# Kernel tuning notes

Measured on AMD Instinct MI355X. Metric: run time of the kernel, lower is better.

The kernel has to match this reference:

```python
import jax, jax.numpy as jnp
import numpy as np

N = 4096
IN_DIM = 8
OUT_DIM = 8
MAX_DEPTH = 8


def _linear_params(key, fan_in, fan_out):
    kw, kb = jax.random.split(key)
    scale = 1.0 / np.sqrt(fan_in)
    W = jax.random.uniform(kw, (fan_in, fan_out), jnp.float32, -scale, scale)
    b = jax.random.uniform(kb, (fan_out,), jnp.float32, -scale, scale)
    return W, b


def setup_inputs() -> dict:
    key = jax.random.key(0)
    ks = jax.random.split(key, 8)
    x = jax.random.normal(ks[0], (N, IN_DIM), jnp.float32)
    # reachability matrices; scaled by 1/N to keep depth iteration stable
    rem = jax.random.uniform(ks[1], (MAX_DEPTH, N, N), jnp.float32) * (1.0 / N)
    pW1, pb1 = _linear_params(ks[2], IN_DIM, 16)
    pW2, pb2 = _linear_params(ks[3], 16, 8)
    pW3, pb3 = _linear_params(ks[4], 8, OUT_DIM)
    aW1, ab1 = _linear_params(ks[5], IN_DIM, 16)
    aW2, ab2 = _linear_params(ks[6], 16, 8)
    aW3, ab3 = _linear_params(ks[7], 8, OUT_DIM)
    return {
        "x": x, "reachable_edge_matrix": rem,
        "pW1": pW1, "pb1": pb1, "pW2": pW2, "pb2": pb2, "pW3": pW3, "pb3": pb3,
        "aW1": aW1, "ab1": ab1, "aW2": aW2, "ab2": ab2, "aW3": aW3, "ab3": ab3,
    }


def _mlp3(h, W1, b1, W2, b2, W3, b3):
    act = jax.nn.leaky_relu
    h = act(h @ W1 + b1)
    h = act(h @ W2 + b2)
    return act(h @ W3 + b3)


def reference(x, reachable_edge_matrix,
              pW1, pb1, pW2, pb2, pW3, pb3,
              aW1, ab1, aW2, ab2, aW3, ab3):
    out0 = _mlp3(x, pW1, pb1, pW2, pb2, pW3, pb3)  # [N, OUT_DIM]

    def step(out, A_d):
        agg = _mlp3(out, aW1, ab1, aW2, ab2, aW3, ab3)
        out = A_d @ agg + out  # [N,N]x[N,OUT_DIM] aggregation
        return out, None

    out, _ = jax.lax.scan(step, out0, reachable_edge_matrix)
    return out
```

## Files before the change

kernel.cpp:

```cpp
#include <hip/hip_runtime.h>

#define NN 4096

__device__ float g_outf[NN*8];
__device__ float g_agg0[NN*8];
__device__ float g_agg1[NN*8];

__device__ __forceinline__ float lrelu(float x){ return x > 0.0f ? x : 0.01f * x; }

__device__ void mlp3(const float* in,
                     const float* W1, const float* b1,
                     const float* W2, const float* b2,
                     const float* W3, const float* b3, float* out)
{
  float h1[16];
  #pragma unroll
  for (int m=0;m<16;m++){
    float s = b1[m];
    #pragma unroll
    for (int k=0;k<8;k++) s += in[k]*W1[k*16+m];
    h1[m] = lrelu(s);
  }
  float h2[8];
  #pragma unroll
  for (int m=0;m<8;m++){
    float s = b2[m];
    #pragma unroll
    for (int k=0;k<16;k++) s += h1[k]*W2[k*8+m];
    h2[m] = lrelu(s);
  }
  #pragma unroll
  for (int c=0;c<8;c++){
    float s = b3[c];
    #pragma unroll
    for (int k=0;k<8;k++) s += h2[k]*W3[k*8+c];
    out[c] = lrelu(s);
  }
}

__global__ __launch_bounds__(256) void init_kernel(
    const float* __restrict__ x,
    const float* pW1,const float* pb1,const float* pW2,const float* pb2,const float* pW3,const float* pb3,
    const float* aW1,const float* ab1,const float* aW2,const float* ab2,const float* aW3,const float* ab3)
{
  int i = blockIdx.x*256 + threadIdx.x;
  float in[8];
  #pragma unroll
  for (int k=0;k<8;k++) in[k] = x[i*8+k];
  float o[8];
  mlp3(in, pW1,pb1,pW2,pb2,pW3,pb3, o);
  #pragma unroll
  for (int c=0;c<8;c++) g_outf[i*8+c] = o[c];
  float a[8];
  mlp3(o, aW1,ab1,aW2,ab2,aW3,ab3, a);
  #pragma unroll
  for (int c=0;c<8;c++) g_agg0[i*8+c] = a[c];
}

__global__ __launch_bounds__(256,1) void agg_update(
    const float* __restrict__ A, int parity, float* __restrict__ finout,
    const float* __restrict__ aW1,const float* __restrict__ ab1,
    const float* __restrict__ aW2,const float* __restrict__ ab2,
    const float* __restrict__ aW3,const float* __restrict__ ab3)
{
  const float* aggin  = parity ? g_agg1 : g_agg0;
  float*       aggout = parity ? g_agg0 : g_agg1;

  const int lane = threadIdx.x & 63;
  const int wav  = threadIdx.x >> 6;
  const int i0   = (blockIdx.x*4 + wav) * 4;

  const float4* Ar0 = reinterpret_cast<const float4*>(A + (size_t)(i0+0)*NN) + lane;
  const float4* Ar1 = reinterpret_cast<const float4*>(A + (size_t)(i0+1)*NN) + lane;
  const float4* Ar2 = reinterpret_cast<const float4*>(A + (size_t)(i0+2)*NN) + lane;
  const float4* Ar3 = reinterpret_cast<const float4*>(A + (size_t)(i0+3)*NN) + lane;
  const float4* gp  = reinterpret_cast<const float4*>(aggin) + (size_t)lane*8;

  float acc[4][8];
  #pragma unroll
  for (int r=0;r<4;r++)
    #pragma unroll
    for (int c=0;c<8;c++) acc[r][c] = 0.0f;

  for (int it=0; it<16; ++it){
    float4 a0 = Ar0[it*64];
    float4 a1 = Ar1[it*64];
    float4 a2 = Ar2[it*64];
    float4 a3 = Ar3[it*64];
    float4 g[8];
    #pragma unroll
    for (int t=0;t<8;t++) g[t] = gp[it*512 + t];

    const float av[4][4] = {{a0.x,a0.y,a0.z,a0.w},
                            {a1.x,a1.y,a1.z,a1.w},
                            {a2.x,a2.y,a2.z,a2.w},
                            {a3.x,a3.y,a3.z,a3.w}};
    #pragma unroll
    for (int jj=0;jj<4;jj++){
      const float gl[8] = {g[2*jj].x, g[2*jj].y, g[2*jj].z, g[2*jj].w,
                           g[2*jj+1].x, g[2*jj+1].y, g[2*jj+1].z, g[2*jj+1].w};
      #pragma unroll
      for (int r=0;r<4;r++){
        const float a = av[r][jj];
        #pragma unroll
        for (int c=0;c<8;c++) acc[r][c] += a*gl[c];
      }
    }
  }

  #pragma unroll
  for (int r=0;r<4;r++)
    #pragma unroll
    for (int c=0;c<8;c++){
      float v = acc[r][c];
      #pragma unroll
      for (int s=1;s<64;s<<=1) v += __shfl_xor(v, s, 64);
      acc[r][c] = v;
    }

  const int r = lane >> 4, m = lane & 15;
  float* po = g_outf + (size_t)i0*8;

  float rowv[8];
  #pragma unroll
  for (int k=0;k<8;k++) rowv[k] = po[r*8+k] + acc[r][k];

  if (lane < 32){
    float t = 0.0f;
    #pragma unroll
    for (int rr=0;rr<4;rr++)
      #pragma unroll
      for (int cc=0;cc<8;cc++)
        if (rr*8+cc == lane) t = acc[rr][cc];
    float sv = po[lane] + t;
    po[lane] = sv;
    if (finout) finout[(size_t)i0*8 + lane] = sv;
  }

  if (!finout){
    float h1 = ab1[m];
    #pragma unroll
    for (int k=0;k<8;k++) h1 += rowv[k]*aW1[k*16+m];
    h1 = lrelu(h1);
    const int m8 = m & 7;
    float s2 = ab2[m8];
    #pragma unroll
    for (int k=0;k<16;k++) s2 += __shfl(h1, (lane & 48)+k, 64) * aW2[k*8+m8];
    float h2 = lrelu(s2);
    float s3 = ab3[m8];
    #pragma unroll
    for (int k=0;k<8;k++) s3 += __shfl(h2, (lane & 48)+k, 64) * aW3[k*8+m8];
    float av = lrelu(s3);
    if (m < 8) aggout[(size_t)(i0+r)*8 + m] = av;
  }
}

extern "C" void kernel_launch(void* const* d_in, const int* in_sizes, int n_in,
                              void* d_out, int out_size, void* d_ws, size_t ws_size,
                              hipStream_t stream)
{
  const float* x   = (const float*)d_in[0];
  const float* rem = (const float*)d_in[1];
  const float* pW1 = (const float*)d_in[2];
  const float* pb1 = (const float*)d_in[3];
  const float* pW2 = (const float*)d_in[4];
  const float* pb2 = (const float*)d_in[5];
  const float* pW3 = (const float*)d_in[6];
  const float* pb3 = (const float*)d_in[7];
  const float* aW1 = (const float*)d_in[8];
  const float* ab1 = (const float*)d_in[9];
  const float* aW2 = (const float*)d_in[10];
  const float* ab2 = (const float*)d_in[11];
  const float* aW3 = (const float*)d_in[12];
  const float* ab3 = (const float*)d_in[13];
  float* outf = (float*)d_out;

  init_kernel<<<16,256,0,stream>>>(x,pW1,pb1,pW2,pb2,pW3,pb3,
                                   aW1,ab1,aW2,ab2,aW3,ab3);
  for (int d=0; d<8; ++d){
    agg_update<<<256,256,0,stream>>>(rem + (size_t)d*NN*NN, (d&1),
                                     (d==7)? outf : (float*)nullptr,
                                     aW1,ab1,aW2,ab2,aW3,ab3);
  }
}
```

Baseline: 828.4 us.

## Fuse init and all depth steps into one persistent kernel with grid barrier

Replaces the init launch plus eight per-depth launches with a single persistent kernel of 256 blocks that synchronises between depth steps through a software sense-reversing grid barrier built on global atomics. It also register-prefetches the next A tile inside the loop and the first tile of the next depth, to hide load latency. This removes launch gaps and pipeline drain between steps. It relies on all 256 blocks being co-resident, otherwise it can deadlock. The barrier spin and fences add their own overhead, and the workload is dominated by streaming the 512MB A matrix from memory.

```diff
diff --git a/kernel.cpp b/kernel.cpp
--- a/kernel.cpp
+++ b/kernel.cpp
@@ -5,6 +5,8 @@
 __device__ float g_outf[NN*8];
 __device__ float g_agg0[NN*8];
 __device__ float g_agg1[NN*8];
+__device__ unsigned g_bar;
+__device__ unsigned g_sense;
 
 __device__ __forceinline__ float lrelu(float x){ return x > 0.0f ? x : 0.01f * x; }
 
@@ -38,120 +40,165 @@
   }
 }
 
-__global__ __launch_bounds__(256) void init_kernel(
-    const float* __restrict__ x,
-    const float* pW1,const float* pb1,const float* pW2,const float* pb2,const float* pW3,const float* pb3,
-    const float* aW1,const float* ab1,const float* aW2,const float* ab2,const float* aW3,const float* ab3)
-{
-  int i = blockIdx.x*256 + threadIdx.x;
-  float in[8];
-  #pragma unroll
-  for (int k=0;k<8;k++) in[k] = x[i*8+k];
-  float o[8];
-  mlp3(in, pW1,pb1,pW2,pb2,pW3,pb3, o);
-  #pragma unroll
-  for (int c=0;c<8;c++) g_outf[i*8+c] = o[c];
-  float a[8];
-  mlp3(o, aW1,ab1,aW2,ab2,aW3,ab3, a);
-  #pragma unroll
-  for (int c=0;c<8;c++) g_agg0[i*8+c] = a[c];
-}
-
-__global__ __launch_bounds__(256,1) void agg_update(
-    const float* __restrict__ A, int parity, float* __restrict__ finout,
+__device__ __forceinline__ void grid_sync()
+{
+  __threadfence();
+  __syncthreads();
+  if (threadIdx.x == 0){
+    unsigned gen = __hip_atomic_load(&g_sense, __ATOMIC_ACQUIRE, __HIP_MEMORY_SCOPE_AGENT);
+    unsigned n   = __hip_atomic_fetch_add(&g_bar, 1u, __ATOMIC_ACQ_REL, __HIP_MEMORY_SCOPE_AGENT);
+    if (n == gridDim.x - 1u){
+      __hip_atomic_store(&g_bar, 0u, __ATOMIC_RELAXED, __HIP_MEMORY_SCOPE_AGENT);
+      __hip_atomic_store(&g_sense, gen + 1u, __ATOMIC_RELEASE, __HIP_MEMORY_SCOPE_AGENT);
+    } else {
+      while (__hip_atomic_load(&g_sense, __ATOMIC_ACQUIRE, __HIP_MEMORY_SCOPE_AGENT) == gen)
+        __builtin_amdgcn_s_sleep(2);
+    }
+  }
+  __syncthreads();
+  __threadfence();
+}
+
+__global__ __launch_bounds__(256,1) void fused_graph(
+    const float* __restrict__ x, const float* __restrict__ rem,
+    float* __restrict__ finout,
+    const float* __restrict__ pW1,const float* __restrict__ pb1,
+    const float* __restrict__ pW2,const float* __restrict__ pb2,
+    const float* __restrict__ pW3,const float* __restrict__ pb3,
     const float* __restrict__ aW1,const float* __restrict__ ab1,
     const float* __restrict__ aW2,const float* __restrict__ ab2,
     const float* __restrict__ aW3,const float* __restrict__ ab3)
 {
-  const float* aggin  = parity ? g_agg1 : g_agg0;
-  float*       aggout = parity ? g_agg0 : g_agg1;
-
   const int lane = threadIdx.x & 63;
   const int wav  = threadIdx.x >> 6;
   const int i0   = (blockIdx.x*4 + wav) * 4;
 
-  const float4* Ar0 = reinterpret_cast<const float4*>(A + (size_t)(i0+0)*NN) + lane;
-  const float4* Ar1 = reinterpret_cast<const float4*>(A + (size_t)(i0+1)*NN) + lane;
-  const float4* Ar2 = reinterpret_cast<const float4*>(A + (size_t)(i0+2)*NN) + lane;
-  const float4* Ar3 = reinterpret_cast<const float4*>(A + (size_t)(i0+3)*NN) + lane;
-  const float4* gp  = reinterpret_cast<const float4*>(aggin) + (size_t)lane*8;
-
-  float acc[4][8];
-  #pragma unroll
-  for (int r=0;r<4;r++)
-    #pragma unroll
-    for (int c=0;c<8;c++) acc[r][c] = 0.0f;
-
-  for (int it=0; it<16; ++it){
-    float4 a0 = Ar0[it*64];
-    float4 a1 = Ar1[it*64];
-    float4 a2 = Ar2[it*64];
-    float4 a3 = Ar3[it*64];
-    float4 g[8];
-    #pragma unroll
-    for (int t=0;t<8;t++) g[t] = gp[it*512 + t];
-
-    const float av[4][4] = {{a0.x,a0.y,a0.z,a0.w},
-                            {a1.x,a1.y,a1.z,a1.w},
-                            {a2.x,a2.y,a2.z,a2.w},
-                            {a3.x,a3.y,a3.z,a3.w}};
-    #pragma unroll
-    for (int jj=0;jj<4;jj++){
-      const float gl[8] = {g[2*jj].x, g[2*jj].y, g[2*jj].z, g[2*jj].w,
-                           g[2*jj+1].x, g[2*jj+1].y, g[2*jj+1].z, g[2*jj+1].w};
-      #pragma unroll
-      for (int r=0;r<4;r++){
-        const float a = av[r][jj];
+  const float4* A0p = reinterpret_cast<const float4*>(rem + (size_t)(i0+0)*NN) + lane;
+  const float4* A1p = reinterpret_cast<const float4*>(rem + (size_t)(i0+1)*NN) + lane;
+  const float4* A2p = reinterpret_cast<const float4*>(rem + (size_t)(i0+2)*NN) + lane;
+  const float4* A3p = reinterpret_cast<const float4*>(rem + (size_t)(i0+3)*NN) + lane;
+
+  float4 nA0 = A0p[0], nA1 = A1p[0], nA2 = A2p[0], nA3 = A3p[0];
+
+  if (blockIdx.x < 16){
+    const int i = blockIdx.x*256 + threadIdx.x;
+    float in[8];
+    #pragma unroll
+    for (int k=0;k<8;k++) in[k] = x[i*8+k];
+    float o[8];
+    mlp3(in, pW1,pb1,pW2,pb2,pW3,pb3, o);
+    #pragma unroll
+    for (int c=0;c<8;c++) g_outf[i*8+c] = o[c];
+    float a[8];
+    mlp3(o, aW1,ab1,aW2,ab2,aW3,ab3, a);
+    #pragma unroll
+    for (int c=0;c<8;c++) g_agg0[i*8+c] = a[c];
+  }
+  grid_sync();
+
+  const size_t DSTEP = (size_t)NN*(NN/4);
+
+  for (int d=0; d<8; ++d){
+    const float* aggin  = (d&1) ? g_agg1 : g_agg0;
+    float*       aggout = (d&1) ? g_agg0 : g_agg1;
+    const float4* gp  = reinterpret_cast<const float4*>(aggin) + (size_t)lane*8;
+    const float4* Ad0 = A0p + (size_t)d*DSTEP;
+    const float4* Ad1 = A1p + (size_t)d*DSTEP;
+    const float4* Ad2 = A2p + (size_t)d*DSTEP;
+    const float4* Ad3 = A3p + (size_t)d*DSTEP;
+
+    float acc[4][8];
+    #pragma unroll
+    for (int r=0;r<4;r++)
+      #pragma unroll
+      for (int c=0;c<8;c++) acc[r][c] = 0.0f;
+
+    float4 cA0=nA0, cA1=nA1, cA2=nA2, cA3=nA3;
+
+    for (int it=0; it<16; ++it){
+      float4 fA0, fA1, fA2, fA3;
+      if (it < 15){
+        fA0 = Ad0[(it+1)*64];
+        fA1 = Ad1[(it+1)*64];
+        fA2 = Ad2[(it+1)*64];
+        fA3 = Ad3[(it+1)*64];
+      }
+      float4 G[8];
+      #pragma unroll
+      for (int t=0;t<8;t++) G[t] = gp[(size_t)it*512 + t];
+
+      const float av[4][4] = {{cA0.x,cA0.y,cA0.z,cA0.w},
+                              {cA1.x,cA1.y,cA1.z,cA1.w},
+                              {cA2.x,cA2.y,cA2.z,cA2.w},
+                              {cA3.x,cA3.y,cA3.z,cA3.w}};
+      #pragma unroll
+      for (int jj=0;jj<4;jj++){
+        const float gl[8] = {G[2*jj].x, G[2*jj].y, G[2*jj].z, G[2*jj].w,
+                             G[2*jj+1].x, G[2*jj+1].y, G[2*jj+1].z, G[2*jj+1].w};
         #pragma unroll
-        for (int c=0;c<8;c++) acc[r][c] += a*gl[c];
+        for (int r=0;r<4;r++){
+          const float a = av[r][jj];
+          #pragma unroll
+          for (int c=0;c<8;c++) acc[r][c] += a*gl[c];
+        }
       }
-    }
-  }
-
-  #pragma unroll
-  for (int r=0;r<4;r++)
-    #pragma unroll
-    for (int c=0;c<8;c++){
-      float v = acc[r][c];
-      #pragma unroll
-      for (int s=1;s<64;s<<=1) v += __shfl_xor(v, s, 64);
-      acc[r][c] = v;
-    }
-
-  const int r = lane >> 4, m = lane & 15;
-  float* po = g_outf + (size_t)i0*8;
-
-  float rowv[8];
-  #pragma unroll
-  for (int k=0;k<8;k++) rowv[k] = po[r*8+k] + acc[r][k];
-
-  if (lane < 32){
-    float t = 0.0f;
-    #pragma unroll
-    for (int rr=0;rr<4;rr++)
-      #pragma unroll
-      for (int cc=0;cc<8;cc++)
-        if (rr*8+cc == lane) t = acc[rr][cc];
-    float sv = po[lane] + t;
-    po[lane] = sv;
-    if (finout) finout[(size_t)i0*8 + lane] = sv;
-  }
-
-  if (!finout){
-    float h1 = ab1[m];
-    #pragma unroll
-    for (int k=0;k<8;k++) h1 += rowv[k]*aW1[k*16+m];
-    h1 = lrelu(h1);
-    const int m8 = m & 7;
-    float s2 = ab2[m8];
-    #pragma unroll
-    for (int k=0;k<16;k++) s2 += __shfl(h1, (lane & 48)+k, 64) * aW2[k*8+m8];
-    float h2 = lrelu(s2);
-    float s3 = ab3[m8];
-    #pragma unroll
-    for (int k=0;k<8;k++) s3 += __shfl(h2, (lane & 48)+k, 64) * aW3[k*8+m8];
-    float av = lrelu(s3);
-    if (m < 8) aggout[(size_t)(i0+r)*8 + m] = av;
+      if (it < 15){ cA0=fA0; cA1=fA1; cA2=fA2; cA3=fA3; }
+    }
+
+    if (d < 7){
+      nA0 = Ad0[DSTEP];
+      nA1 = Ad1[DSTEP];
+      nA2 = Ad2[DSTEP];
+      nA3 = Ad3[DSTEP];
+    }
+
+    #pragma unroll
+    for (int r=0;r<4;r++)
+      #pragma unroll
+      for (int c=0;c<8;c++){
+        float v = acc[r][c];
+        #pragma unroll
+        for (int s=1;s<64;s<<=1) v += __shfl_xor(v, s, 64);
+        acc[r][c] = v;
+      }
+
+    const int r = lane >> 4, m = lane & 15;
+    float* po = g_outf + (size_t)i0*8;
+
+    float rowv[8];
+    #pragma unroll
+    for (int k=0;k<8;k++) rowv[k] = po[r*8+k] + acc[r][k];
+
+    if (lane < 32){
+      float t = 0.0f;
+      #pragma unroll
+      for (int rr=0;rr<4;rr++)
+        #pragma unroll
+        for (int cc=0;cc<8;cc++)
+          if (rr*8+cc == lane) t = acc[rr][cc];
+      float sv = po[lane] + t;
+      po[lane] = sv;
+      if (d == 7) finout[(size_t)i0*8 + lane] = sv;
+    }
+
+    if (d < 7){
+      float h1 = ab1[m];
+      #pragma unroll
+      for (int k=0;k<8;k++) h1 += rowv[k]*aW1[k*16+m];
+      h1 = lrelu(h1);
+      const int m8 = m & 7;
+      float s2 = ab2[m8];
+      #pragma unroll
+      for (int k=0;k<16;k++) s2 += __shfl(h1, (lane & 48)+k, 64) * aW2[k*8+m8];
+      float h2 = lrelu(s2);
+      float s3 = ab3[m8];
+      #pragma unroll
+      for (int k=0;k<8;k++) s3 += __shfl(h2, (lane & 48)+k, 64) * aW3[k*8+m8];
+      float av2 = lrelu(s3);
+      if (m < 8) aggout[(size_t)(i0+r)*8 + m] = av2;
+
+      grid_sync();
+    }
   }
 }
 
@@ -175,11 +222,7 @@
   const float* ab3 = (const float*)d_in[13];
   float* outf = (float*)d_out;
 
-  init_kernel<<<16,256,0,stream>>>(x,pW1,pb1,pW2,pb2,pW3,pb3,
-                                   aW1,ab1,aW2,ab2,aW3,ab3);
-  for (int d=0; d<8; ++d){
-    agg_update<<<256,256,0,stream>>>(rem + (size_t)d*NN*NN, (d&1),
-                                     (d==7)? outf : (float*)nullptr,
-                                     aW1,ab1,aW2,ab2,aW3,ab3);
-  }
-}
+  fused_graph<<<256,256,0,stream>>>(x, rem, outf,
+                                    pW1,pb1,pW2,pb2,pW3,pb3,
+                                    aW1,ab1,aW2,ab2,aW3,ab3);
+}
```

After: 1.217 ms. 1.47x slower.

## Halve rows per wave, double grid, and software-prefetch A and agg loads

Applied to the files above, without the earlier changes.

Each wave now handles 2 rows of A instead of 4, and the grid doubles to 512 blocks, so more waves are in flight to stream the memory-bound A matrix. The inner loop adds explicit register double-buffering: A is prefetched two iterations ahead and agg one iteration ahead, to hide load latency. In exchange the agg vector is re-read twice as often per A row, and register pressure rises from the prefetch buffers. The MLP epilogue is adjusted so only the lanes for the two rows write outputs.

```diff
diff --git a/kernel.cpp b/kernel.cpp
--- a/kernel.cpp
+++ b/kernel.cpp
@@ -57,7 +57,7 @@
   for (int c=0;c<8;c++) g_agg0[i*8+c] = a[c];
 }
 
-__global__ __launch_bounds__(256,1) void agg_update(
+__global__ __launch_bounds__(256,2) void agg_update(
     const float* __restrict__ A, int parity, float* __restrict__ finout,
     const float* __restrict__ aW1,const float* __restrict__ ab1,
     const float* __restrict__ aW2,const float* __restrict__ ab2,
@@ -68,48 +68,60 @@
 
   const int lane = threadIdx.x & 63;
   const int wav  = threadIdx.x >> 6;
-  const int i0   = (blockIdx.x*4 + wav) * 4;
+  const int i0   = (blockIdx.x*4 + wav) * 2;
 
   const float4* Ar0 = reinterpret_cast<const float4*>(A + (size_t)(i0+0)*NN) + lane;
   const float4* Ar1 = reinterpret_cast<const float4*>(A + (size_t)(i0+1)*NN) + lane;
-  const float4* Ar2 = reinterpret_cast<const float4*>(A + (size_t)(i0+2)*NN) + lane;
-  const float4* Ar3 = reinterpret_cast<const float4*>(A + (size_t)(i0+3)*NN) + lane;
   const float4* gp  = reinterpret_cast<const float4*>(aggin) + (size_t)lane*8;
 
-  float acc[4][8];
+  float acc[2][8];
   #pragma unroll
-  for (int r=0;r<4;r++)
+  for (int r=0;r<2;r++)
     #pragma unroll
     for (int c=0;c<8;c++) acc[r][c] = 0.0f;
 
+  float4 cA0 = Ar0[0],  cA1 = Ar1[0];
+  float4 nA0 = Ar0[64], nA1 = Ar1[64];
+  float4 cG[8];
+  #pragma unroll
+  for (int t=0;t<8;t++) cG[t] = gp[t];
+
   for (int it=0; it<16; ++it){
-    float4 a0 = Ar0[it*64];
-    float4 a1 = Ar1[it*64];
-    float4 a2 = Ar2[it*64];
-    float4 a3 = Ar3[it*64];
-    float4 g[8];
-    #pragma unroll
-    for (int t=0;t<8;t++) g[t] = gp[it*512 + t];
+    float4 pA0, pA1;
+    if (it < 14){
+      pA0 = Ar0[(it+2)*64];
+      pA1 = Ar1[(it+2)*64];
+    }
+    float4 fG[8];
+    if (it < 15){
+      #pragma unroll
+      for (int t=0;t<8;t++) fG[t] = gp[(it+1)*512 + t];
+    }
 
-    const float av[4][4] = {{a0.x,a0.y,a0.z,a0.w},
-                            {a1.x,a1.y,a1.z,a1.w},
-                            {a2.x,a2.y,a2.z,a2.w},
-                            {a3.x,a3.y,a3.z,a3.w}};
+    const float av[2][4] = {{cA0.x,cA0.y,cA0.z,cA0.w},
+                            {cA1.x,cA1.y,cA1.z,cA1.w}};
     #pragma unroll
     for (int jj=0;jj<4;jj++){
-      const float gl[8] = {g[2*jj].x, g[2*jj].y, g[2*jj].z, g[2*jj].w,
-                           g[2*jj+1].x, g[2*jj+1].y, g[2*jj+1].z, g[2*jj+1].w};
+      const float gl[8] = {cG[2*jj].x, cG[2*jj].y, cG[2*jj].z, cG[2*jj].w,
+                           cG[2*jj+1].x, cG[2*jj+1].y, cG[2*jj+1].z, cG[2*jj+1].w};
       #pragma unroll
-      for (int r=0;r<4;r++){
+      for (int r=0;r<2;r++){
         const float a = av[r][jj];
         #pragma unroll
         for (int c=0;c<8;c++) acc[r][c] += a*gl[c];
       }
     }
+
+    cA0 = nA0; cA1 = nA1;
+    if (it < 14){ nA0 = pA0; nA1 = pA1; }
+    if (it < 15){
+      #pragma unroll
+      for (int t=0;t<8;t++) cG[t] = fG[t];
+    }
   }
 
   #pragma unroll
-  for (int r=0;r<4;r++)
+  for (int r=0;r<2;r++)
     #pragma unroll
     for (int c=0;c<8;c++){
       float v = acc[r][c];
@@ -118,17 +130,17 @@
       acc[r][c] = v;
     }
 
-  const int r = lane >> 4, m = lane & 15;
+  const int r = (lane >> 4) & 1, m = lane & 15;
   float* po = g_outf + (size_t)i0*8;
 
   float rowv[8];
   #pragma unroll
-  for (int k=0;k<8;k++) rowv[k] = po[r*8+k] + acc[r][k];
+  for (int k=0;k<8;k++) rowv[k] = po[r*8+k] + (r ? acc[1][k] : acc[0][k]);
 
-  if (lane < 32){
+  if (lane < 16){
     float t = 0.0f;
     #pragma unroll
-    for (int rr=0;rr<4;rr++)
+    for (int rr=0;rr<2;rr++)
       #pragma unroll
       for (int cc=0;cc<8;cc++)
         if (rr*8+cc == lane) t = acc[rr][cc];
@@ -150,8 +162,8 @@
     float s3 = ab3[m8];
     #pragma unroll
     for (int k=0;k<8;k++) s3 += __shfl(h2, (lane & 48)+k, 64) * aW3[k*8+m8];
-    float av = lrelu(s3);
-    if (m < 8) aggout[(size_t)(i0+r)*8 + m] = av;
+    float av2 = lrelu(s3);
+    if (m < 8 && lane < 32) aggout[(size_t)(i0+r)*8 + m] = av2;
   }
 }
 
@@ -178,7 +190,7 @@
   init_kernel<<<16,256,0,stream>>>(x,pW1,pb1,pW2,pb2,pW3,pb3,
                                    aW1,ab1,aW2,ab2,aW3,ab3);
   for (int d=0; d<8; ++d){
-    agg_update<<<256,256,0,stream>>>(rem + (size_t)d*NN*NN, (d&1),
+    agg_update<<<512,256,0,stream>>>(rem + (size_t)d*NN*NN, (d&1),
                                      (d==7)? outf : (float*)nullptr,
                                      aW1,ab1,aW2,ab2,aW3,ab3);
   }
```

Result: slower. 1.027 ms (+24.0%).
